# Performance work log

Hardware: AMD Instinct MI355X
Metric: run time of the kernel (lower is better)

Reference implementation:

```python
import jax, jax.numpy as jnp
import numpy as np

EMBED_DIM = 512
NUM_HEADS = 8
HEAD_DIM = EMBED_DIM // NUM_HEADS
B, N, M = 4, 4096, 4096


def setup_inputs() -> dict:
    key = jax.random.key(0)
    ks = jax.random.split(key, 16)
    s = 0.02
    inp = {
        "query": jax.random.normal(ks[0], (B, N, EMBED_DIM), jnp.float32),
        "key": jax.random.normal(ks[1], (B, M, EMBED_DIM), jnp.float32),
        "value": jax.random.normal(ks[2], (B, M, EMBED_DIM), jnp.float32),
        # Linear weights stored as (in, out) so y = x @ W + b (== torch x @ W.T + b)
        "Wq": jax.random.normal(ks[3], (EMBED_DIM, EMBED_DIM), jnp.float32) * s,
        "bq": jnp.zeros((EMBED_DIM,), jnp.float32),
        "Wk": jax.random.normal(ks[4], (EMBED_DIM, EMBED_DIM), jnp.float32) * s,
        "bk": jnp.zeros((EMBED_DIM,), jnp.float32),
        "Wv": jax.random.normal(ks[5], (EMBED_DIM, EMBED_DIM), jnp.float32) * s,
        "bv": jnp.zeros((EMBED_DIM,), jnp.float32),
        # rank expansion MLP acts per-head on head_dim
        "W1": jax.random.normal(ks[6], (HEAD_DIM, HEAD_DIM * 2), jnp.float32) * s,
        "b1": jnp.zeros((HEAD_DIM * 2,), jnp.float32),
        "W2": jax.random.normal(ks[7], (HEAD_DIM * 2, HEAD_DIM), jnp.float32) * s,
        "b2": jnp.zeros((HEAD_DIM,), jnp.float32),
        "Wo": jax.random.normal(ks[8], (EMBED_DIM, EMBED_DIM), jnp.float32) * s,
        "bo": jnp.zeros((EMBED_DIM,), jnp.float32),
    }
    return inp


def reference(query, key, value, Wq, bq, Wk, bk, Wv, bv, W1, b1, W2, b2, Wo, bo):
    b, n, _ = query.shape
    m = key.shape[1]
    H, D = NUM_HEADS, HEAD_DIM
    # ELU+1 feature maps on projected q, k
    q = jax.nn.elu(query @ Wq + bq) + 1.0           # [B,N,E]
    k = jax.nn.elu(key @ Wk + bk) + 1.0             # [B,M,E]
    v = value @ Wv + bv                              # [B,M,E]
    q = q.reshape(b, n, H, D)
    k = k.reshape(b, m, H, D)
    v = v.reshape(b, m, H, D)
    # rank expansion MLP on keys (per head_dim), exact GELU as nn.GELU default
    k_aug = jax.nn.gelu(k @ W1 + b1, approximate=False) @ W2 + b2
    k_aug = jax.nn.elu(k_aug) + 1.0                  # [B,M,H,D]
    # inputs already fp32 (torch .float() casts are identity here)
    k_scaled = k_aug / m                             # normalize over context len
    kv_context = jnp.einsum('bmhd,bmhe->bhde', k_scaled, v)   # [B,H,D,D]
    out = jnp.einsum('bnhd,bhde->bnhe', q, kv_context)        # [B,N,H,D]
    k_sum = k_scaled.sum(axis=1)                      # [B,H,D]
    denom = jnp.einsum('bnhd,bhd->bnh', q, k_sum)     # [B,N,H]
    out = out / jnp.clip(denom, 1e-6, None)[..., None]
    out = jnp.clip(jnp.nan_to_num(out, nan=0.0, posinf=65000.0, neginf=-65000.0),
                   -65000.0, 65000.0)
    out = out.reshape(b, n, H * D)
    return out @ Wo + bo
```

## Files before the change

kernel.cpp:

```cpp
#include <hip/hip_runtime.h>
#include <hip/hip_bf16.h>
#include <cmath>

#define DEV __device__ __forceinline__

typedef __bf16 bf16x8 __attribute__((ext_vector_type(8)));
typedef float f32x4 __attribute__((ext_vector_type(4)));
typedef unsigned int u32;
typedef unsigned short u16;

#define S_VMCNT(N) asm volatile("s_waitcnt vmcnt(" #N ")" ::: "memory")
#define S_LGKM0    asm volatile("s_waitcnt lgkmcnt(0)" ::: "memory")
#define S_FENCE    asm volatile("" ::: "memory")
#define S_BAR      __builtin_amdgcn_s_barrier()

DEV u16 f2bf(float f) {
  union { float f; u32 u; } v;
  v.f = f;
  u32 u = v.u;
  u += 0x7fffu + ((u >> 16) & 1u);
  return (u16)(u >> 16);
}
DEV u32 pk2(float a, float b) {
  union { __hip_bfloat162 h2; u32 u; } v;
  v.h2 = __float22bfloat162_rn(float2{a, b});
  return v.u;
}

DEV void async16(const void* g, void* l) {
  __builtin_amdgcn_global_load_lds((const __attribute__((address_space(1))) u32*)g,
                                   (__attribute__((address_space(3))) u32*)l, 16, 0, 0);
}

DEV int swz(int row, int kq) { return row * 64 + ((kq * 8) ^ ((row & 7) << 3)); }

__global__ __launch_bounds__(256, 2)
void qkv_gemm(const float* __restrict__ qin, const float* __restrict__ kin,
              const float* __restrict__ vin, const u16* __restrict__ WqP,
              const u16* __restrict__ WkP, const u16* __restrict__ WvP,
              const float* __restrict__ bq, const float* __restrict__ bk,
              const float* __restrict__ bv, const u16* __restrict__ W1T,
              const u16* __restrict__ W2T, const float* __restrict__ b1,
              const float* __restrict__ b2, u16* __restrict__ qact,
              u16* __restrict__ vT, u16* __restrict__ kaT, float invM)
{
  __shared__ __align__(16) u16 SB[32768];

  const int z = blockIdx.z;
  const float* Af = z == 0 ? qin : z == 1 ? kin : vin;
  const u16* Bp = z == 0 ? WqP : z == 1 ? WkP : WvP;
  const float* bias = z == 0 ? bq : z == 1 ? bk : bv;

  const int tid = threadIdx.x, wv = tid >> 6, lane = tid & 63;
  const int wr = wv >> 1, wc = wv & 1;
  const int lrow = lane & 15, lq = lane >> 4;
  const long r0 = (long)blockIdx.x * 128;
  const int c0 = blockIdx.y * 128;

  f32x4 acc[4][4] = {};
  float4 rA[2][8];

  auto loadA = [&](float4* dst, int T) {
#pragma unroll
    for (int it = 0; it < 4; ++it) {
      const int s = it * 256 + tid;
      const int row = s >> 3, kq = s & 7;
      const float* g = Af + (r0 + row) * 512 + T * 64 + kq * 8;
      dst[2 * it]     = *(const float4*)g;
      dst[2 * it + 1] = *(const float4*)(g + 4);
    }
  };
  auto cvtStoreA = [&](const float4* src, u16* bufA) {
#pragma unroll
    for (int it = 0; it < 4; ++it) {
      const int s = it * 256 + tid;
      const int row = s >> 3, kq = s & 7;
      union { u32 q[4]; uint4 v; } pk;
      pk.q[0] = pk2(src[2 * it].x, src[2 * it].y);
      pk.q[1] = pk2(src[2 * it].z, src[2 * it].w);
      pk.q[2] = pk2(src[2 * it + 1].x, src[2 * it + 1].y);
      pk.q[3] = pk2(src[2 * it + 1].z, src[2 * it + 1].w);
      *(uint4*)&bufA[swz(row, kq)] = pk.v;
    }
  };
  auto issueB = [&](int T, u16* bufB) {
#pragma unroll
    for (int it = 0; it < 4; ++it) {
      const int sl = it * 256 + wv * 64;
      async16(Bp + ((long)blockIdx.y * 8 + T) * 8192 + (sl + lane) * 8, &bufB[sl * 8]);
    }
  };
  auto computeT = [&](const u16* Ac, const u16* Bc) {
#pragma unroll
    for (int subk = 0; subk < 2; ++subk) {
      bf16x8 af[4], bfr[4];
#pragma unroll
      for (int i = 0; i < 4; ++i)
        af[i] = *(const bf16x8*)&Ac[swz(wr * 64 + i * 16 + lrow, subk * 4 + lq)];
#pragma unroll
      for (int j = 0; j < 4; ++j)
        bfr[j] = *(const bf16x8*)&Bc[swz(wc * 64 + j * 16 + lrow, subk * 4 + lq)];
#pragma unroll
      for (int i = 0; i < 4; ++i)
#pragma unroll
        for (int j = 0; j < 4; ++j)
          acc[i][j] = __builtin_amdgcn_mfma_f32_16x16x32_bf16(af[i], bfr[j], acc[i][j], 0, 0, 0);
    }
  };

  issueB(0, SB + 8192);
  S_FENCE;
  loadA(rA[0], 0);
  loadA(rA[1], 1);
  cvtStoreA(rA[0], SB);
  S_LGKM0;
  S_VMCNT(8);
  S_BAR;

#pragma unroll
  for (int t = 0; t < 8; ++t) {
    const int cur = t & 1, nxt = 1 - cur;
    u16* Ac = SB + cur * 16384;
    u16* Bc = Ac + 8192;
    u16* An = SB + nxt * 16384;
    u16* Bn = An + 8192;
    if (t < 7) issueB(t + 1, Bn);
    S_FENCE;
    if (t < 6) loadA(rA[cur], t + 2);
    if (t < 7) cvtStoreA(rA[nxt], An);
    computeT(Ac, Bc);
    S_LGKM0;
    if (t < 6)       { S_VMCNT(8); }
    else if (t == 6) { S_VMCNT(0); }
    S_BAR;
  }

  if (z == 0) {
#pragma unroll
    for (int i = 0; i < 4; ++i) {
#pragma unroll
      for (int j = 0; j < 4; ++j) {
        const int col = c0 + wc * 64 + j * 16 + lrow;
        const float bvv = bias[col];
#pragma unroll
        for (int p = 0; p < 4; ++p) {
          float o = acc[i][j][p] + bvv;
          o = (o > 0.f) ? (o + 1.f) : __expf(o);
          const long row = r0 + wr * 64 + i * 16 + lq * 4 + p;
          qact[row * 512 + col] = f2bf(o);
        }
      }
    }
  } else if (z == 2) {
    u16* LTv = SB + wv * 4608;
#pragma unroll
    for (int i = 0; i < 4; ++i) {
#pragma unroll
      for (int j = 0; j < 4; ++j) {
        const int col = c0 + wc * 64 + j * 16 + lrow;
        const float bvv = bias[col];
        ushort4 w;
        w.x = f2bf(acc[i][j][0] + bvv);
        w.y = f2bf(acc[i][j][1] + bvv);
        w.z = f2bf(acc[i][j][2] + bvv);
        w.w = f2bf(acc[i][j][3] + bvv);
        *(ushort4*)&LTv[(j * 16 + lrow) * 72 + i * 16 + lq * 4] = w;
      }
    }
    const int b = (int)(r0 >> 12);
    const int h = (c0 + wc * 64) >> 6;
    const int mg0 = (int)(r0 & 4095) + wr * 64;
    __syncthreads();
#pragma unroll
    for (int ps = 0; ps < 8; ++ps) {
      const int e = ps * 8 + (lane >> 3);
      const int mq = (lane & 7) * 8;
      uint4 v = *(const uint4*)&LTv[e * 72 + mq];
      *(uint4*)(vT + (((long)b * 8 + h) * 64 + e) * 4096 + mg0 + mq) = v;
    }
  } else {
    u16* As_k = SB;
    u16* hid  = SB + 16384;
    const int b   = (int)(r0 >> 12);
    const int m0g = (int)(r0 & 4095);
    const int h0  = c0 >> 6;

#pragma unroll
    for (int i = 0; i < 4; ++i)
#pragma unroll
      for (int j = 0; j < 4; ++j) {
        const int col = c0 + wc * 64 + j * 16 + lrow;
        const float bvv = bias[col];
        const int d = j * 16 + lrow;
#pragma unroll
        for (int p = 0; p < 4; ++p) {
          const int m = wr * 64 + i * 16 + lq * 4 + p;
          float o = acc[i][j][p] + bvv;
          o = (o > 0.f) ? (o + 1.f) : __expf(o);
          As_k[wc * 8192 + m * 64 + ((((d >> 3) ^ (m & 7)) << 3) | (d & 7))] = f2bf(o);
        }
      }
    __syncthreads();

    const int c0m = (wv >> 1) * 64, mh0 = (wv & 1) * 64;
    const int d0  = (wv >> 1) * 32, mh2 = (wv & 1) * 64;

    for (int hh = 0; hh < 2; ++hh) {
      f32x4 acc1[4][4] = {};
#pragma unroll
      for (int kt = 0; kt < 2; ++kt) {
        bf16x8 wa[4], kb[4];
#pragma unroll
        for (int i = 0; i < 4; ++i)
          wa[i] = *(const bf16x8*)(W1T + (c0m + i * 16 + lrow) * 64 + kt * 32 + lq * 8);
#pragma unroll
        for (int j = 0; j < 4; ++j) {
          const int m = mh0 + j * 16 + lrow;
          kb[j] = *(const bf16x8*)&As_k[hh * 8192 + m * 64 + (((kt * 4 + lq) ^ (m & 7)) << 3)];
        }
#pragma unroll
        for (int i = 0; i < 4; ++i)
#pragma unroll
          for (int j = 0; j < 4; ++j)
            acc1[i][j] = __builtin_amdgcn_mfma_f32_16x16x32_bf16(wa[i], kb[j], acc1[i][j], 0, 0, 0);
      }

#pragma unroll
      for (int i = 0; i < 4; ++i) {
        const int cc = c0m + i * 16 + lq * 4;
        float4 bv4 = *(const float4*)(b1 + cc);
#pragma unroll
        for (int j = 0; j < 4; ++j) {
          const int m = mh0 + j * 16 + lrow;
          float x0 = acc1[i][j][0] + bv4.x, x1 = acc1[i][j][1] + bv4.y;
          float x2 = acc1[i][j][2] + bv4.z, x3 = acc1[i][j][3] + bv4.w;
          ushort4 w;
          w.x = f2bf(0.5f * x0 * (1.f + erff(x0 * 0.7071067811865475f)));
          w.y = f2bf(0.5f * x1 * (1.f + erff(x1 * 0.7071067811865475f)));
          w.z = f2bf(0.5f * x2 * (1.f + erff(x2 * 0.7071067811865475f)));
          w.w = f2bf(0.5f * x3 * (1.f + erff(x3 * 0.7071067811865475f)));
          *(ushort4*)&hid[m * 128 + ((((cc >> 3) ^ (m & 7)) << 3) | (cc & 7))] = w;
        }
      }
      __syncthreads();

      f32x4 acc2[4][2] = {};
#pragma unroll
      for (int kt = 0; kt < 4; ++kt) {
        bf16x8 wa2[2], hb[4];
#pragma unroll
        for (int i = 0; i < 2; ++i)
          wa2[i] = *(const bf16x8*)(W2T + (d0 + i * 16 + lrow) * 128 + kt * 32 + lq * 8);
#pragma unroll
        for (int j = 0; j < 4; ++j) {
          const int m = mh2 + j * 16 + lrow;
          hb[j] = *(const bf16x8*)&hid[m * 128 + (((kt * 4 + lq) ^ (m & 7)) << 3)];
        }
#pragma unroll
        for (int j = 0; j < 4; ++j)
#pragma unroll
          for (int i = 0; i < 2; ++i)
            acc2[j][i] = __builtin_amdgcn_mfma_f32_16x16x32_bf16(hb[j], wa2[i], acc2[j][i], 0, 0, 0);
      }

      u16* LT2 = SB + hh * 8192;
#pragma unroll
      for (int i = 0; i < 2; ++i) {
        const int d = d0 + i * 16 + lrow;
        const float bd = b2[d];
#pragma unroll
        for (int j = 0; j < 4; ++j) {
          const int ml = mh2 + j * 16 + lq * 4;
          ushort4 w;
#pragma unroll
          for (int p = 0; p < 4; ++p) {
            float v = acc2[j][i][p] + bd;
            v = ((v > 0.f) ? (v + 1.f) : __expf(v)) * invM;
            ((u16*)&w)[p] = f2bf(v);
          }
          *(ushort4*)&LT2[d * 128 + ((((ml >> 3) ^ (d & 7)) << 3) | (ml & 7))] = w;
        }
      }
      __syncthreads();

      const int bh2 = b * 8 + h0 + hh;
#pragma unroll
      for (int it = 0; it < 4; ++it) {
        const int u = it * 256 + tid;
        const int mo = u & 15, hd = u >> 4;
        uint4 v = *(const uint4*)&LT2[hd * 128 + ((mo ^ (hd & 7)) << 3)];
        *(uint4*)(kaT + ((long)bh2 * 64 + hd) * 4096 + m0g + mo * 8) = v;
      }
    }
  }
}

__global__ __launch_bounds__(256, 2)
void out_gemm(const u16* __restrict__ A, const u16* __restrict__ Bt,
              const float* __restrict__ bias, float* __restrict__ Y)
{
  __shared__ __align__(16) u16 SB[32768];
  const int tid = threadIdx.x, wv = tid >> 6, lane = tid & 63;
  const int wr = wv >> 1, wc = wv & 1;
  const int lrow = lane & 15, lq = lane >> 4;
  const long r0 = (long)blockIdx.x * 128;
  const int c0 = blockIdx.y * 128;

  auto stage = [&](int T, u16* buf) {
#pragma unroll
    for (int it = 0; it < 4; ++it) {
      const int sl = it * 256 + wv * 64;
      async16(A  + ((long)blockIdx.x * 8 + T) * 8192 + (sl + lane) * 8, &buf[sl * 8]);
      async16(Bt + ((long)blockIdx.y * 8 + T) * 8192 + (sl + lane) * 8, &buf[8192 + sl * 8]);
    }
  };

  f32x4 acc[4][4] = {};
  stage(0, SB);
  S_VMCNT(0);
  S_BAR;

#pragma unroll
  for (int t = 0; t < 8; ++t) {
    const int cur = t & 1, nxt = 1 - cur;
    if (t < 7) stage(t + 1, SB + nxt * 16384);
    const u16* Ac = SB + cur * 16384;
    const u16* Bc = Ac + 8192;
#pragma unroll
    for (int subk = 0; subk < 2; ++subk) {
      bf16x8 af[4], bfr[4];
#pragma unroll
      for (int i = 0; i < 4; ++i)
        af[i] = *(const bf16x8*)&Ac[swz(wr * 64 + i * 16 + lrow, subk * 4 + lq)];
#pragma unroll
      for (int j = 0; j < 4; ++j)
        bfr[j] = *(const bf16x8*)&Bc[swz(wc * 64 + j * 16 + lrow, subk * 4 + lq)];
#pragma unroll
      for (int i = 0; i < 4; ++i)
#pragma unroll
        for (int j = 0; j < 4; ++j)
          acc[i][j] = __builtin_amdgcn_mfma_f32_16x16x32_bf16(af[i], bfr[j], acc[i][j], 0, 0, 0);
    }
    S_LGKM0;
    if (t < 7) { S_VMCNT(0); }
    S_BAR;
  }
#pragma unroll
  for (int i = 0; i < 4; ++i) {
#pragma unroll
    for (int j = 0; j < 4; ++j) {
      const int col = c0 + wc * 64 + j * 16 + lrow;
      const float bv = bias[col];
#pragma unroll
      for (int p = 0; p < 4; ++p) {
        const long row = r0 + wr * 64 + i * 16 + lq * 4 + p;
        Y[row * 512 + col] = acc[i][j][p] + bv;
      }
    }
  }
}

struct TArgs {
  const float* src[6];
  u16* dst[6];
  int K[6];
  int N[6];
};
__global__ __launch_bounds__(256)
void transpose_w(TArgs a)
{
  const int m = blockIdx.z;
  const int K = a.K[m], N = a.N[m];
  const int kt = blockIdx.y * 64, nt = blockIdx.x * 64;
  if (kt >= K || nt >= N) return;
  const float* src = a.src[m];
  u16* dst = a.dst[m];
  __shared__ u16 t[64][72];
  const int tx = threadIdx.x & 15, ty = threadIdx.x >> 4;
#pragma unroll
  for (int rr = 0; rr < 64; rr += 16) {
    const int k = kt + ty + rr;
    float4 v = *(const float4*)(src + (long)k * N + nt + tx * 4);
    t[tx * 4 + 0][ty + rr] = f2bf(v.x);
    t[tx * 4 + 1][ty + rr] = f2bf(v.y);
    t[tx * 4 + 2][ty + rr] = f2bf(v.z);
    t[tx * 4 + 3][ty + rr] = f2bf(v.w);
  }
  __syncthreads();
  if (m < 4) {
    const int ktile = kt >> 6;
#pragma unroll
    for (int it = 0; it < 2; ++it) {
      const int s = threadIdx.x + it * 256;
      const int r = s >> 3, c = (s & 7) * 8;
      const int n = nt + r;
      const int colblk = n >> 7, cl = n & 127;
      ushort4 u0 = *(ushort4*)&t[r][c];
      ushort4 u1 = *(ushort4*)&t[r][c + 4];
      u16* d = dst + ((long)colblk * 8 + ktile) * 8192 + cl * 64 + (c ^ ((cl & 7) << 3));
      *(ushort4*)d = u0;
      *(ushort4*)(d + 4) = u1;
    }
  } else {
#pragma unroll
    for (int it = 0; it < 2; ++it) {
      const int s = threadIdx.x + it * 256;
      const int r = s >> 3, c = (s & 7) * 8;
      ushort4 u0 = *(ushort4*)&t[r][c];
      ushort4 u1 = *(ushort4*)&t[r][c + 4];
      *(ushort4*)(dst + (long)(nt + r) * K + kt + c) = u0;
      *(ushort4*)(dst + (long)(nt + r) * K + kt + c + 4) = u1;
    }
  }
}

__global__ __launch_bounds__(256, 2)
void kv_gemm(const u16* __restrict__ kaT, const u16* __restrict__ vT,
             float* __restrict__ kvp, float* __restrict__ ksp)
{
  const int sp = blockIdx.x;
  const int bh = blockIdx.y;
  __shared__ __align__(16) u16 SB[32768];
  const int tid = threadIdx.x, wv = tid >> 6, lane = tid & 63;
  const int lrow = lane & 15, lq = lane >> 4;
  f32x4 acc[4][4] = {};
  f32x4 accs[4] = {};
  bf16x8 ones;
#pragma unroll
  for (int z = 0; z < 8; ++z) ones[z] = (__bf16)1.0f;
  const long base = (long)bh * 64 * 4096;

#pragma unroll
  for (int ph = 0; ph < 2; ++ph) {
    const int m0 = sp * 256 + ph * 128;
#pragma unroll
    for (int i = 0; i < 4; ++i) {
      const int s = (wv * 4 + i) * 64 + lane;
      const int chunk = s >> 8, row = (s >> 2) & 63, part = s & 3;
      const long g = base + (long)row * 4096 + m0 + chunk * 32 + part * 8;
      async16(kaT + g, &SB[ph * 16384 + (wv * 4 + i) * 512]);
      async16(vT + g, &SB[ph * 16384 + 8192 + (wv * 4 + i) * 512]);
    }
    S_FENCE;
  }

#pragma unroll
  for (int ph = 0; ph < 2; ++ph) {
    if (ph == 0) { S_VMCNT(8); } else { S_VMCNT(0); }
    const u16* As = SB + ph * 16384;
    const u16* Bs = As + 8192;
    bf16x8 af[4], bfr[4];
#pragma unroll
    for (int i = 0; i < 4; ++i)
      af[i] = *(const bf16x8*)&As[wv * 2048 + (i * 16 + lrow) * 32 + lq * 8];
#pragma unroll
    for (int j = 0; j < 4; ++j)
      bfr[j] = *(const bf16x8*)&Bs[wv * 2048 + (j * 16 + lrow) * 32 + lq * 8];
#pragma unroll
    for (int i = 0; i < 4; ++i) {
#pragma unroll
      for (int j = 0; j < 4; ++j)
        acc[i][j] = __builtin_amdgcn_mfma_f32_16x16x32_bf16(af[i], bfr[j], acc[i][j], 0, 0, 0);
      accs[i] = __builtin_amdgcn_mfma_f32_16x16x32_bf16(af[i], ones, accs[i], 0, 0, 0);
    }
  }

  float* red = (float*)SB;
  float* ksr = red + 64 * 68;
  for (int w = 0; w < 4; ++w) {
    __syncthreads();
    if (wv == w) {
#pragma unroll
      for (int i = 0; i < 4; ++i) {
#pragma unroll
        for (int j = 0; j < 4; ++j) {
          const int e = j * 16 + lrow, dd = i * 16 + lq * 4;
          float* p = &red[e * 68 + dd];
          if (w == 0) { p[0] = acc[i][j][0]; p[1] = acc[i][j][1]; p[2] = acc[i][j][2]; p[3] = acc[i][j][3]; }
          else        { p[0] += acc[i][j][0]; p[1] += acc[i][j][1]; p[2] += acc[i][j][2]; p[3] += acc[i][j][3]; }
        }
        if (lrow == 0) {
          const int dd = i * 16 + lq * 4;
#pragma unroll
          for (int p2 = 0; p2 < 4; ++p2) {
            if (w == 0) ksr[dd + p2] = accs[i][p2];
            else        ksr[dd + p2] += accs[i][p2];
          }
        }
      }
    }
  }
  __syncthreads();
  float* kvo = kvp + ((long)sp * 32 + bh) * 4096;
  for (int s = tid; s < 4096; s += 256) kvo[s] = red[(s >> 6) * 68 + (s & 63)];
  if (tid < 64) ksp[(sp * 32 + bh) * 64 + tid] = ksr[tid];
}

__global__ __launch_bounds__(256)
void kv_reduce(const float* __restrict__ kvp, const float* __restrict__ ksp,
               u16* __restrict__ kvT, u16* __restrict__ ksumT)
{
  const int bh = blockIdx.x;
  const int t = threadIdx.x;
  const int s0 = blockIdx.y * 512;
#pragma unroll
  for (int i = 0; i < 2; ++i) {
    const int s = s0 + i * 256 + t;
    float v = 0.f;
#pragma unroll
    for (int sp = 0; sp < 16; ++sp) v += kvp[((long)sp * 32 + bh) * 4096 + s];
    kvT[(long)bh * 4096 + s] = f2bf(v);
  }
  if (blockIdx.y == 0 && t < 64) {
    float v = 0.f;
#pragma unroll
    for (int sp = 0; sp < 16; ++sp) v += ksp[(sp * 32 + bh) * 64 + t];
    ksumT[bh * 64 + t] = f2bf(v);
  }
}

__global__ __launch_bounds__(256)
void attn_mfma(const u16* __restrict__ q, const u16* __restrict__ kvT,
               const u16* __restrict__ ksumT, u16* __restrict__ attn)
{
  __shared__ u16 SB[17408];
  const int tid = threadIdx.x, wv = tid >> 6, lane = tid & 63;
  const int lrow = lane & 15, lq = lane >> 4;
  const int n0 = blockIdx.x * 256;
  const int bh = blockIdx.y, b = bh >> 3, h = bh & 7;
  u16* As = SB;

#pragma unroll
  for (int half = 0; half < 2; ++half)
#pragma unroll
    for (int i = 0; i < 4; ++i) {
      const int s = (wv * 4 + i) * 64 + lane;
      async16(q + ((long)(b * 4096 + n0 + (s >> 2))) * 512 + h * 64 + half * 32 + (s & 3) * 8,
              &As[half * 8192 + (wv * 4 + i) * 512]);
    }
  bf16x8 bfr[2][4], ks[2];
#pragma unroll
  for (int half = 0; half < 2; ++half) {
#pragma unroll
    for (int j = 0; j < 4; ++j)
      bfr[half][j] = *(const bf16x8*)(kvT + ((long)bh * 64 + j * 16 + lrow) * 64 + half * 32 + lq * 8);
    ks[half] = *(const bf16x8*)(ksumT + bh * 64 + half * 32 + lq * 8);
  }
  __syncthreads();

  f32x4 acc[4][4] = {};
  f32x4 accd[4] = {};
#pragma unroll
  for (int half = 0; half < 2; ++half) {
    bf16x8 af[4];
#pragma unroll
    for (int i = 0; i < 4; ++i)
      af[i] = *(const bf16x8*)&As[half * 8192 + (wv * 64 + i * 16 + lrow) * 32 + lq * 8];
#pragma unroll
    for (int i = 0; i < 4; ++i) {
#pragma unroll
      for (int j = 0; j < 4; ++j)
        acc[i][j] = __builtin_amdgcn_mfma_f32_16x16x32_bf16(af[i], bfr[half][j], acc[i][j], 0, 0, 0);
      accd[i] = __builtin_amdgcn_mfma_f32_16x16x32_bf16(af[i], ks[half], accd[i], 0, 0, 0);
    }
  }
  __syncthreads();

  u16* LT = SB;
#pragma unroll
  for (int i = 0; i < 4; ++i) {
    float dinv[4];
#pragma unroll
    for (int p = 0; p < 4; ++p) dinv[p] = 1.f / fmaxf(accd[i][p], 1e-6f);
#pragma unroll
    for (int j = 0; j < 4; ++j) {
      const int e = j * 16 + lrow;
      const int nl0 = i * 16 + lq * 4;
      ushort4 w;
      float x0 = acc[i][j][0] * dinv[0], x1 = acc[i][j][1] * dinv[1];
      float x2 = acc[i][j][2] * dinv[2], x3 = acc[i][j][3] * dinv[3];
      if (!(x0 == x0)) x0 = 0.f;
      if (!(x1 == x1)) x1 = 0.f;
      if (!(x2 == x2)) x2 = 0.f;
      if (!(x3 == x3)) x3 = 0.f;
      w.x = f2bf(fminf(65000.f, fmaxf(-65000.f, x0)));
      w.y = f2bf(fminf(65000.f, fmaxf(-65000.f, x1)));
      w.z = f2bf(fminf(65000.f, fmaxf(-65000.f, x2)));
      w.w = f2bf(fminf(65000.f, fmaxf(-65000.f, x3)));
      *(ushort4*)&LT[wv * 4352 + e * 68 + nl0] = w;
    }
  }
  __syncthreads();
#pragma unroll
  for (int it = 0; it < 8; ++it) {
    const int c = it * 256 + tid;
    const int n = c & 255, ec = c >> 8;
    const int wr2 = n >> 6, nl = n & 63;
    ushort4 w0, w1;
    w0.x = LT[wr2 * 4352 + (ec * 8 + 0) * 68 + nl];
    w0.y = LT[wr2 * 4352 + (ec * 8 + 1) * 68 + nl];
    w0.z = LT[wr2 * 4352 + (ec * 8 + 2) * 68 + nl];
    w0.w = LT[wr2 * 4352 + (ec * 8 + 3) * 68 + nl];
    w1.x = LT[wr2 * 4352 + (ec * 8 + 4) * 68 + nl];
    w1.y = LT[wr2 * 4352 + (ec * 8 + 5) * 68 + nl];
    w1.z = LT[wr2 * 4352 + (ec * 8 + 6) * 68 + nl];
    w1.w = LT[wr2 * 4352 + (ec * 8 + 7) * 68 + nl];
    const int ng = b * 4096 + n0 + n;
    const int rowblk = ng >> 7, rl = ng & 127;
    u16* dst = attn + ((long)rowblk * 8 + h) * 8192 + rl * 64 + ((ec * 8) ^ ((rl & 7) << 3));
    *(ushort4*)dst = w0;
    *(ushort4*)(dst + 4) = w1;
  }
}

static constexpr long U = 8388608;

extern "C" void kernel_launch(void* const* d_in, const int* in_sizes, int n_in,
                              void* d_out, int out_size, void* d_ws, size_t ws_size,
                              hipStream_t stream)
{
  const float* query = (const float*)d_in[0];
  const float* key   = (const float*)d_in[1];
  const float* value = (const float*)d_in[2];
  const float* Wq = (const float*)d_in[3];
  const float* bq = (const float*)d_in[4];
  const float* Wk = (const float*)d_in[5];
  const float* bk = (const float*)d_in[6];
  const float* Wv = (const float*)d_in[7];
  const float* bv = (const float*)d_in[8];
  const float* W1 = (const float*)d_in[9];
  const float* b1 = (const float*)d_in[10];
  const float* W2 = (const float*)d_in[11];
  const float* b2 = (const float*)d_in[12];
  const float* Wo = (const float*)d_in[13];
  const float* bo = (const float*)d_in[14];

  u16* wsh = (u16*)d_ws;
  u16* qact = wsh;
  u16* vT   = wsh + 2 * U;
  u16* kaT  = wsh + 3 * U;
  u16* attn = wsh + 4 * U;

  float* fp  = (float*)(wsh + 5 * U);
  float* kvp = fp;
  float* ksp = fp + 2097152;
  u16* kvTg   = (u16*)(fp + 2129920);
  u16* ksumTg = kvTg + 131072;
  u16* wtb = ksumTg + 2048;
  u16* WqT = wtb;
  u16* WkT = wtb + 262144;
  u16* WvT = wtb + 524288;
  u16* WoT = wtb + 786432;
  u16* W1T = wtb + 1048576;
  u16* W2T = wtb + 1056768;

  dim3 blk(256);
  const float invM = 1.f / 4096.f;

  TArgs ta;
  ta.src[0] = Wq; ta.dst[0] = WqT; ta.K[0] = 512; ta.N[0] = 512;
  ta.src[1] = Wk; ta.dst[1] = WkT; ta.K[1] = 512; ta.N[1] = 512;
  ta.src[2] = Wv; ta.dst[2] = WvT; ta.K[2] = 512; ta.N[2] = 512;
  ta.src[3] = Wo; ta.dst[3] = WoT; ta.K[3] = 512; ta.N[3] = 512;
  ta.src[4] = W1; ta.dst[4] = W1T; ta.K[4] = 64;  ta.N[4] = 128;
  ta.src[5] = W2; ta.dst[5] = W2T; ta.K[5] = 128; ta.N[5] = 64;
  transpose_w<<<dim3(8, 8, 6), blk, 0, stream>>>(ta);

  qkv_gemm<<<dim3(128, 4, 3), blk, 0, stream>>>(query, key, value, WqT, WkT, WvT,
                                                bq, bk, bv, W1T, W2T, b1, b2,
                                                qact, vT, kaT, invM);
  kv_gemm<<<dim3(16, 32), blk, 0, stream>>>(kaT, vT, kvp, ksp);
  kv_reduce<<<dim3(32, 8), blk, 0, stream>>>(kvp, ksp, kvTg, ksumTg);
  attn_mfma<<<dim3(16, 32), blk, 0, stream>>>(qact, kvTg, ksumTg, attn);
  out_gemm<<<dim3(128, 4), blk, 0, stream>>>(attn, WoT, bo, (float*)d_out);
}
```

Before: 249.3 us.

## Pre-convert QKV inputs to swizzled bf16 tiles and stage both operands asynchronously

Adds a prep kernel that converts the fp32 query/key/value activations to bf16 in the swizzled tile layout the GEMM expects. The QKV GEMM then loads both A and B tiles with direct global-to-LDS async loads instead of register loads followed by conversion and an LDS store. This removes per-tile conversion work and register pressure from the GEMM, at the cost of an extra kernel launch and an extra pass that writes and rereads a bf16 copy of the inputs. Scratch buffers overlap existing workspace regions and the output buffer, and the pipeline now waits for all outstanding loads (vmcnt 0) on every iteration.

```diff
diff --git a/kernel.cpp b/kernel.cpp
--- a/kernel.cpp
+++ b/kernel.cpp
@@ -34,9 +34,34 @@
 
 DEV int swz(int row, int kq) { return row * 64 + ((kq * 8) ^ ((row & 7) << 3)); }
 
+__global__ __launch_bounds__(256)
+void prep_qkv(const float* __restrict__ qin, const float* __restrict__ kin,
+              const float* __restrict__ vin, u16* __restrict__ qb,
+              u16* __restrict__ kb, u16* __restrict__ vb)
+{
+  const int z = blockIdx.y;
+  const float* src = z == 0 ? qin : z == 1 ? kin : vin;
+  u16* dst = z == 0 ? qb : z == 1 ? kb : vb;
+  const long r0 = (long)blockIdx.x * 64;
+  const int tid = threadIdx.x;
+#pragma unroll 4
+  for (int it = 0; it < 16; ++it) {
+    const int g = it * 256 + tid;
+    const int rloc = g >> 6, kt = (g >> 3) & 7, kq = g & 7;
+    const long ng = r0 + rloc;
+    const int rb = (int)(ng >> 7), rl = (int)(ng & 127);
+    const float* s = src + ng * 512 + kt * 64 + kq * 8;
+    float4 lo = *(const float4*)s, hi = *(const float4*)(s + 4);
+    union { u32 q[4]; uint4 v; } pk;
+    pk.q[0] = pk2(lo.x, lo.y); pk.q[1] = pk2(lo.z, lo.w);
+    pk.q[2] = pk2(hi.x, hi.y); pk.q[3] = pk2(hi.z, hi.w);
+    *(uint4*)(dst + ((long)rb * 8 + kt) * 8192 + rl * 64 + ((kq * 8) ^ ((rl & 7) << 3))) = pk.v;
+  }
+}
+
 __global__ __launch_bounds__(256, 2)
-void qkv_gemm(const float* __restrict__ qin, const float* __restrict__ kin,
-              const float* __restrict__ vin, const u16* __restrict__ WqP,
+void qkv_gemm(const u16* __restrict__ qbI, const u16* __restrict__ kbI,
+              const u16* __restrict__ vbI, const u16* __restrict__ WqP,
               const u16* __restrict__ WkP, const u16* __restrict__ WvP,
               const float* __restrict__ bq, const float* __restrict__ bk,
               const float* __restrict__ bv, const u16* __restrict__ W1T,
@@ -47,7 +72,7 @@
   __shared__ __align__(16) u16 SB[32768];
 
   const int z = blockIdx.z;
-  const float* Af = z == 0 ? qin : z == 1 ? kin : vin;
+  const u16* Ai = z == 0 ? qbI : z == 1 ? kbI : vbI;
   const u16* Bp = z == 0 ? WqP : z == 1 ? WkP : WvP;
   const float* bias = z == 0 ? bq : z == 1 ? bk : bv;
 
@@ -57,40 +82,26 @@
   const long r0 = (long)blockIdx.x * 128;
   const int c0 = blockIdx.y * 128;
 
-  f32x4 acc[4][4] = {};
-  float4 rA[2][8];
-
-  auto loadA = [&](float4* dst, int T) {
-#pragma unroll
-    for (int it = 0; it < 4; ++it) {
-      const int s = it * 256 + tid;
-      const int row = s >> 3, kq = s & 7;
-      const float* g = Af + (r0 + row) * 512 + T * 64 + kq * 8;
-      dst[2 * it]     = *(const float4*)g;
-      dst[2 * it + 1] = *(const float4*)(g + 4);
-    }
-  };
-  auto cvtStoreA = [&](const float4* src, u16* bufA) {
-#pragma unroll
-    for (int it = 0; it < 4; ++it) {
-      const int s = it * 256 + tid;
-      const int row = s >> 3, kq = s & 7;
-      union { u32 q[4]; uint4 v; } pk;
-      pk.q[0] = pk2(src[2 * it].x, src[2 * it].y);
-      pk.q[1] = pk2(src[2 * it].z, src[2 * it].w);
-      pk.q[2] = pk2(src[2 * it + 1].x, src[2 * it + 1].y);
-      pk.q[3] = pk2(src[2 * it + 1].z, src[2 * it + 1].w);
-      *(uint4*)&bufA[swz(row, kq)] = pk.v;
-    }
-  };
-  auto issueB = [&](int T, u16* bufB) {
+  auto stage = [&](int T, u16* buf) {
 #pragma unroll
     for (int it = 0; it < 4; ++it) {
       const int sl = it * 256 + wv * 64;
-      async16(Bp + ((long)blockIdx.y * 8 + T) * 8192 + (sl + lane) * 8, &bufB[sl * 8]);
+      async16(Ai + ((long)blockIdx.x * 8 + T) * 8192 + (sl + lane) * 8, &buf[sl * 8]);
+      async16(Bp + ((long)blockIdx.y * 8 + T) * 8192 + (sl + lane) * 8, &buf[8192 + sl * 8]);
     }
   };
-  auto computeT = [&](const u16* Ac, const u16* Bc) {
+
+  f32x4 acc[4][4] = {};
+  stage(0, SB);
+  S_VMCNT(0);
+  S_BAR;
+
+#pragma unroll
+  for (int t = 0; t < 8; ++t) {
+    const int cur = t & 1, nxt = 1 - cur;
+    if (t < 7) stage(t + 1, SB + nxt * 16384);
+    const u16* Ac = SB + cur * 16384;
+    const u16* Bc = Ac + 8192;
 #pragma unroll
     for (int subk = 0; subk < 2; ++subk) {
       bf16x8 af[4], bfr[4];
@@ -106,32 +117,8 @@
         for (int j = 0; j < 4; ++j)
           acc[i][j] = __builtin_amdgcn_mfma_f32_16x16x32_bf16(af[i], bfr[j], acc[i][j], 0, 0, 0);
     }
-  };
-
-  issueB(0, SB + 8192);
-  S_FENCE;
-  loadA(rA[0], 0);
-  loadA(rA[1], 1);
-  cvtStoreA(rA[0], SB);
-  S_LGKM0;
-  S_VMCNT(8);
-  S_BAR;
-
-#pragma unroll
-  for (int t = 0; t < 8; ++t) {
-    const int cur = t & 1, nxt = 1 - cur;
-    u16* Ac = SB + cur * 16384;
-    u16* Bc = Ac + 8192;
-    u16* An = SB + nxt * 16384;
-    u16* Bn = An + 8192;
-    if (t < 7) issueB(t + 1, Bn);
-    S_FENCE;
-    if (t < 6) loadA(rA[cur], t + 2);
-    if (t < 7) cvtStoreA(rA[nxt], An);
-    computeT(Ac, Bc);
     S_LGKM0;
-    if (t < 6)       { S_VMCNT(8); }
-    else if (t == 6) { S_VMCNT(0); }
+    if (t < 7) { S_VMCNT(0); }
     S_BAR;
   }
 
@@ -185,6 +172,7 @@
     const int m0g = (int)(r0 & 4095);
     const int h0  = c0 >> 6;
 
+    __syncthreads();
 #pragma unroll
     for (int i = 0; i < 4; ++i)
 #pragma unroll
@@ -637,9 +625,12 @@
 
   u16* wsh = (u16*)d_ws;
   u16* qact = wsh;
+  u16* qb   = wsh + U;
   u16* vT   = wsh + 2 * U;
   u16* kaT  = wsh + 3 * U;
   u16* attn = wsh + 4 * U;
+  u16* vb   = wsh + 4 * U;
+  u16* kb   = (u16*)d_out;
 
   float* fp  = (float*)(wsh + 5 * U);
   float* kvp = fp;
@@ -666,7 +657,9 @@
   ta.src[5] = W2; ta.dst[5] = W2T; ta.K[5] = 128; ta.N[5] = 64;
   transpose_w<<<dim3(8, 8, 6), blk, 0, stream>>>(ta);
 
-  qkv_gemm<<<dim3(128, 4, 3), blk, 0, stream>>>(query, key, value, WqT, WkT, WvT,
+  prep_qkv<<<dim3(256, 3), blk, 0, stream>>>(query, key, value, qb, kb, vb);
+
+  qkv_gemm<<<dim3(128, 4, 3), blk, 0, stream>>>(qb, kb, vb, WqT, WkT, WvT,
                                                 bq, bk, bv, W1T, W2T, b1, b2,
                                                 qact, vT, kaT, invM);
   kv_gemm<<<dim3(16, 32), blk, 0, stream>>>(kaT, vT, kvp, ksp);
```

Result: slower. 264.4 us (+6.0%).
